# Kernel optimization log

Measured on AMD Instinct MI355X. Metric: run time of the kernel, lower is better.

The kernel has to match this reference:

```python
import jax, jax.numpy as jnp
import numpy as np

H = 512      # hidden_dim
K = 3        # conv_kernel_size
CHUNK = 3    # chunk_size
EPS = 1e-5   # BatchNorm eps


def conv1d(x, w, b, pad):
    # x: (B, Cin, L), w: (Cout, Cin, K)
    y = jax.lax.conv_general_dilated(x, w, (1,), [(pad, pad)],
                                     dimension_numbers=("NCH", "OIH", "NCH"))
    return y + b[None, :, None]


def chunk_indices(seq_lens):
    # static int metadata -> numpy index build (loop over small fixed batch only)
    sl = np.asarray(seq_lens)
    bidx, sidx = [], []
    for b, l in enumerate(sl):
        starts = np.arange(0, int(l) - CHUNK + 1, CHUNK)
        bidx.append(np.full(starts.shape[0], b, dtype=np.int32))
        sidx.append(starts.astype(np.int32))
    return np.concatenate(bidx), np.concatenate(sidx)


def setup_inputs() -> dict:
    key = jax.random.key(0)
    ks = jax.random.split(key, 8)
    B, L = 32, 4096
    x = jax.random.normal(ks[0], (B, L), jnp.float32)
    seq_lens = jax.random.randint(ks[1], (B,), 2048, L + 1)

    def w(k, shape):
        return jax.random.normal(k, shape, jnp.float32) * 0.05

    return {
        "x": x,
        "w0": w(ks[2], (H, 1, K)), "b0": jnp.zeros((H,)), "g0": jnp.ones((H,)), "be0": jnp.zeros((H,)),
        "w1": w(ks[3], (H, H, K)), "b1": jnp.zeros((H,)), "g1": jnp.ones((H,)), "be1": jnp.zeros((H,)),
        "w2": w(ks[4], (H, H, K)), "b2": jnp.zeros((H,)), "g2": jnp.ones((H,)), "be2": jnp.zeros((H,)),
        "pw": w(ks[5], (H, H, CHUNK)), "pb": jnp.zeros((H,)),
        "fw": w(ks[6], (1, H)), "fb": jnp.zeros((1,)),
        "seq_lens": seq_lens,
    }


def reference(x, w0, b0, g0, be0, w1, b1, g1, be1, w2, b2, g2, be2,
              pw, pb, fw, fb, seq_lens):
    inv = np.float32(1.0 / np.sqrt(1.0 + EPS))  # BN eval: mean=0, var=1
    h = x[:, None, :]  # (B, 1, L)
    for (w, b, g, be) in ((w0, b0, g0, be0), (w1, b1, g1, be1), (w2, b2, g2, be2)):
        h = jax.nn.relu(conv1d(h, w, b, pad=1))
        h = (g * inv)[None, :, None] * h + be[None, :, None]
    h = jnp.transpose(h, (0, 2, 1))  # (B, L, H)

    bidx_np, sidx_np = chunk_indices(seq_lens)
    bidx = jnp.asarray(bidx_np)
    sidx = jnp.asarray(sidx_np)
    offs = jnp.arange(CHUNK, dtype=jnp.int32)
    chunks = h[bidx[:, None], sidx[:, None] + offs[None, :], :]  # (N, CHUNK, H)

    # pre_fc_conv over a length-CHUNK window == one GEMM per chunk
    z = jnp.einsum("nth,cht->nc", chunks, pw) + pb  # (N, H)
    logits = jax.nn.relu(z) @ fw.T + fb             # (N, 1)
    return jax.nn.sigmoid(logits)[:, 0]             # (N,)
```

## Files before the change

### kernel.cpp

```cpp
#include <hip/hip_runtime.h>

#define HCH 512
#define LSEQ 4096
#define NB 32
#define KW 3
#define KDIM 1536
#define SPAD 1408
#define INVS 0.9999950000374997f

typedef __attribute__((ext_vector_type(8))) short bf16x8;
typedef __attribute__((ext_vector_type(4))) float f32x4;

__device__ inline unsigned short f2bf(float f) {
  unsigned int u = __float_as_uint(f);
  u += 0x7fffu + ((u >> 16) & 1u);
  return (unsigned short)(u >> 16);
}

__device__ inline void gl_lds16(const void* g, void* l) {
  __builtin_amdgcn_global_load_lds(
      (const __attribute__((address_space(1))) void*)g,
      (__attribute__((address_space(3))) void*)l, 16, 0, 0);
}

__global__ void prep_all(const float* __restrict__ w1, const float* __restrict__ w2,
                         const float* __restrict__ pw, unsigned short* __restrict__ wt,
                         const int* __restrict__ seq_lens, int* __restrict__ cum,
                         float* __restrict__ pz, int nz) {
  int idx = blockIdx.x * 256 + threadIdx.x;
  if (idx < nz) pz[idx] = 0.f;
  if (idx == 0) {
    int acc = 0;
    for (int b = 0; b < NB; b++) {
      cum[b] = acc;
      acc += (seq_lens[b] - KW) / KW + 1;
    }
  }
  if (idx < 3 * HCH * KDIM) {
    int which = idx / (HCH * KDIM);
    int r = idx % (HCH * KDIM);
    int c = r / KDIM;
    int rem = r % KDIM;
    int k = rem / HCH, ci = rem % HCH;
    const float* src = (which == 0) ? w1 : ((which == 1) ? w2 : pw);
    wt[idx] = f2bf(src[c * KDIM + ci * KW + k]);
  }
}

__global__ void layer0(const float* __restrict__ x, const float* __restrict__ w0,
                       const float* __restrict__ b0, const float* __restrict__ g0,
                       const float* __restrict__ be0, unsigned short* __restrict__ h0,
                       const int* __restrict__ seq_q) {
  int tid = threadIdx.x;
  int wave = tid >> 6, lane = tid & 63;
  int pos0 = (blockIdx.x * 4 + wave) * 8;
  int l0 = pos0 & (LSEQ - 1);
  if (l0 >= seq_q[pos0 >> 12] + 2) return;
  int c0 = lane * 8;

  float w[24], bb[8], gg[8], ee[8];
  for (int v = 0; v < 6; v++)
    *reinterpret_cast<float4*>(w + v * 4) = *reinterpret_cast<const float4*>(w0 + c0 * 3 + v * 4);
  for (int v = 0; v < 2; v++) {
    *reinterpret_cast<float4*>(bb + v * 4) = *reinterpret_cast<const float4*>(b0 + c0 + v * 4);
    *reinterpret_cast<float4*>(gg + v * 4) = *reinterpret_cast<const float4*>(g0 + c0 + v * 4);
    *reinterpret_cast<float4*>(ee + v * 4) = *reinterpret_cast<const float4*>(be0 + c0 + v * 4);
  }
  for (int c = 0; c < 8; c++) gg[c] *= INVS;

  const float* xb = x + (size_t)(pos0 - l0);
  for (int pp = 0; pp < 8; pp++) {
    int l = l0 + pp;
    float xm1 = (l > 0) ? xb[l - 1] : 0.f;
    float xc = xb[l];
    float xp1 = (l < LSEQ - 1) ? xb[l + 1] : 0.f;
    unsigned int o[4];
    for (int pq = 0; pq < 4; pq++) {
      unsigned int lo = 0, hi = 0;
      for (int s = 0; s < 2; s++) {
        int c = pq * 2 + s;
        float y = w[c * 3] * xm1 + w[c * 3 + 1] * xc + w[c * 3 + 2] * xp1 + bb[c];
        y = fmaxf(y, 0.f);
        unsigned int u = f2bf(gg[c] * y + ee[c]);
        if (s == 0) lo = u; else hi = u;
      }
      o[pq] = lo | (hi << 16);
    }
    uint4 v4; v4.x = o[0]; v4.y = o[1]; v4.z = o[2]; v4.w = o[3];
    *reinterpret_cast<uint4*>(h0 + (size_t)(pos0 + pp) * HCH + c0) = v4;
  }
}

__global__ __launch_bounds__(256, 2) void conv_gemm(
    const unsigned short* __restrict__ hin,
    const unsigned short* __restrict__ wT,
    const float* __restrict__ bconv, const float* __restrict__ g,
    const float* __restrict__ be,
    unsigned short* __restrict__ hout,
    const unsigned short* __restrict__ zp,
    const int* __restrict__ seq_q, int margin) {
  __shared__ unsigned short As[3 * 128 * 32];
  __shared__ unsigned short Bs[272 * 32];

  int tid = threadIdx.x;
  int wave = tid >> 6, lane = tid & 63;
  int cm = blockIdx.x * 128;
  int ntile = blockIdx.y;
  int b = ntile >> 4;
  int l0 = (ntile & 15) << 8;
  int limit = seq_q[b] + margin;
  if (l0 >= limit) return;
  int wn = wave * 64;
  const size_t hb = (size_t)b * LSEQ * HCH;

  f32x4 acc[8][4] = {};

  int lr = lane >> 2;
  int lc = (lane & 3) * 8;

  const unsigned short* bptr[4];
  for (int t = 0; t < 4; t++) {
    int p = l0 - 1 + (wave * 4 + t) * 16 + lr;
    bptr[t] = (p >= 0 && p < LSEQ) ? (hin + hb + (size_t)p * HCH + lc) : (zp + lc);
  }
  const unsigned short* hptr = zp + lc;
  if (wave == 3 && lane < 8) {
    int p = l0 + 255 + lr;
    hptr = (p < LSEQ) ? (hin + hb + (size_t)p * HCH + lc) : (zp + lc);
  }

  const unsigned short* aptr[6];
  unsigned aoff[6];
  for (int t = 0; t < 6; t++) {
    int s = wave * 6 + t;
    int k = s >> 3, c8 = s & 7;
    aptr[t] = wT + (size_t)(cm + c8 * 16 + lr) * KDIM + k * HCH + lc;
    aoff[t] = (unsigned)(k * 4096 + c8 * 512) * 2;
  }

  for (int it = 0; it < 16; it++) {
    int ci0 = it * 32;
    for (int t = 0; t < 6; t++)
      gl_lds16(aptr[t] + ci0, (char*)As + aoff[t]);
    for (int t = 0; t < 4; t++)
      gl_lds16(bptr[t] + ci0, (char*)Bs + (wave * 4 + t) * 1024);
    if (wave == 3)
      gl_lds16(hptr + ci0, (char*)Bs + 256 * 64);
    __syncthreads();

    int quad = lane >> 4, mr = lane & 15;
    for (int k = 0; k < 3; k++) {
      bf16x8 af[8], bfr[4];
      for (int i = 0; i < 8; i++)
        af[i] = *reinterpret_cast<const bf16x8*>(As + k * 4096 + (i * 16 + mr) * 32 + quad * 8);
      for (int j = 0; j < 4; j++)
        bfr[j] = *reinterpret_cast<const bf16x8*>(Bs + (wn + j * 16 + mr + k) * 32 + quad * 8);
      for (int i = 0; i < 8; i++)
        for (int j = 0; j < 4; j++)
          acc[i][j] = __builtin_amdgcn_mfma_f32_16x16x32_bf16(af[i], bfr[j], acc[i][j], 0, 0, 0);
    }
    __syncthreads();
  }

  int quad = lane >> 4, nn = lane & 15;
  for (int i = 0; i < 8; i++) {
    int c = cm + i * 16 + quad * 4;
    f32x4 bc = *reinterpret_cast<const f32x4*>(bconv + c);
    f32x4 gg = *reinterpret_cast<const f32x4*>(g + c);
    f32x4 bb = *reinterpret_cast<const f32x4*>(be + c);
    for (int j = 0; j < 4; j++) {
      int n = l0 + wn + j * 16 + nn;
      if (n >= limit) continue;
      unsigned long long pack = 0;
      for (int r = 0; r < 4; r++) {
        float y = acc[i][j][r] + bc[r];
        y = fmaxf(y, 0.f);
        unsigned long long u = f2bf(gg[r] * INVS * y + bb[r]);
        pack |= u << (16 * r);
      }
      *reinterpret_cast<unsigned long long*>(hout + hb + (size_t)n * HCH + c) = pack;
    }
  }
}

__global__ __launch_bounds__(256) void chunk_gemm(
    const unsigned short* __restrict__ h2,
    const unsigned short* __restrict__ wTp,
    const float* __restrict__ pb, const float* __restrict__ fw,
    const int* __restrict__ seq_q,
    const int* __restrict__ cum_q,
    float* __restrict__ partial,
    const unsigned short* __restrict__ zp) {
  __shared__ unsigned short As[3 * 128 * 32];
  __shared__ unsigned short Bs[384 * 32];

  int tid = threadIdx.x;
  int wave = tid >> 6, lane = tid & 63;
  int cm = blockIdx.x * 128;
  int b = blockIdx.y / (SPAD / 128);
  int s_base = (blockIdx.y % (SPAD / 128)) * 128;
  int slen = seq_q[b];
  if (3 * s_base + KW > slen) return;
  int p_base = 3 * s_base;
  int wm = (wave >> 1) * 64;
  int wn = (wave & 1) * 64;
  const size_t hb = (size_t)b * LSEQ * HCH;

  f32x4 acc[4][4] = {};

  int lr = lane >> 2, lc = (lane & 3) * 8;

  const unsigned short* bptr[6];
  const unsigned short* aptr[6];
  unsigned aoff[6];
  for (int t = 0; t < 6; t++) {
    int c = wave * 6 + t;
    int p = p_base + c * 16 + lr;
    bptr[t] = (p < LSEQ) ? (h2 + hb + (size_t)p * HCH + lc) : (zp + lc);
    int k = c >> 3, c8 = c & 7;
    aptr[t] = wTp + (size_t)(cm + c8 * 16 + lr) * KDIM + k * HCH + lc;
    aoff[t] = (unsigned)(k * 4096 + c8 * 512) * 2;
  }

  for (int it = 0; it < 16; it++) {
    int ci0 = it * 32;
    for (int t = 0; t < 6; t++) {
      gl_lds16(aptr[t] + ci0, (char*)As + aoff[t]);
      gl_lds16(bptr[t] + ci0, (char*)Bs + (wave * 6 + t) * 1024);
    }
    __syncthreads();

    int quad = lane >> 4, mr = lane & 15;
    for (int t = 0; t < 3; t++) {
      bf16x8 af[4], bfr[4];
      for (int i = 0; i < 4; i++)
        af[i] = *reinterpret_cast<const bf16x8*>(As + t * 4096 + (wm + i * 16 + mr) * 32 + quad * 8);
      for (int j = 0; j < 4; j++)
        bfr[j] = *reinterpret_cast<const bf16x8*>(Bs + (3 * (wn + j * 16 + mr) + t) * 32 + quad * 8);
      for (int i = 0; i < 4; i++)
        for (int j = 0; j < 4; j++)
          acc[i][j] = __builtin_amdgcn_mfma_f32_16x16x32_bf16(af[i], bfr[j], acc[i][j], 0, 0, 0);
    }
    __syncthreads();
  }

  int quad = lane >> 4, nn = lane & 15;
  for (int j = 0; j < 4; j++) {
    float s = 0.f;
    for (int i = 0; i < 4; i++) {
      int c = cm + wm + i * 16 + quad * 4;
      f32x4 pbv = *reinterpret_cast<const f32x4*>(pb + c);
      f32x4 fwv = *reinterpret_cast<const f32x4*>(fw + c);
      for (int r = 0; r < 4; r++) {
        float z = acc[i][j][r] + pbv[r];
        z = fmaxf(z, 0.f);
        s += z * fwv[r];
      }
    }
    s += __shfl_xor(s, 16, 64);
    s += __shfl_xor(s, 32, 64);
    if (quad == 0) {
      int sc = s_base + wn + j * 16 + nn;
      if (3 * sc + KW <= slen) atomicAdd(partial + cum_q[b] + sc, s);
    }
  }
}

__global__ void finalize(const float* __restrict__ partial, const float* __restrict__ fb,
                         float* __restrict__ out, int n) {
  int i = blockIdx.x * 256 + threadIdx.x;
  if (i < n) {
    float t = partial[i] + fb[0];
    out[i] = 1.f / (1.f + expf(-t));
  }
}

extern "C" void kernel_launch(void* const* d_in, const int* in_sizes, int n_in,
                              void* d_out, int out_size, void* d_ws, size_t ws_size,
                              hipStream_t stream) {
  (void)in_sizes; (void)n_in;
  const float* x   = (const float*)d_in[0];
  const float* w0  = (const float*)d_in[1];
  const float* b0  = (const float*)d_in[2];
  const float* g0  = (const float*)d_in[3];
  const float* be0 = (const float*)d_in[4];
  const float* w1  = (const float*)d_in[5];
  const float* b1  = (const float*)d_in[6];
  const float* g1  = (const float*)d_in[7];
  const float* be1 = (const float*)d_in[8];
  const float* w2  = (const float*)d_in[9];
  const float* b2  = (const float*)d_in[10];
  const float* g2  = (const float*)d_in[11];
  const float* be2 = (const float*)d_in[12];
  const float* pw  = (const float*)d_in[13];
  const float* pb  = (const float*)d_in[14];
  const float* fw  = (const float*)d_in[15];
  const float* fb  = (const float*)d_in[16];
  const int* seq_lens = (const int*)d_in[17];

  char* ws = (char*)d_ws;
  unsigned short* zeropage = (unsigned short*)ws;
  float* partial = (float*)(ws + 4096);
  size_t off = 4096 + (size_t)out_size * 4;
  off = (off + 255) & ~(size_t)255;
  int* cum = (int*)(ws + off);
  off += NB * 4;
  off = (off + 255) & ~(size_t)255;
  unsigned short* wt = (unsigned short*)(ws + off);
  off += (size_t)3 * HCH * KDIM * 2;
  off = (off + 255) & ~(size_t)255;
  size_t fixed = off;

  const size_t per_batch = (size_t)LSEQ * HCH * 2;
  int nb_pass = NB;
  while (nb_pass > 1 && fixed + 2 * per_batch * (size_t)nb_pass > ws_size)
    nb_pass >>= 1;
  unsigned short* h0 = (unsigned short*)(ws + fixed);
  unsigned short* h1 = h0 + (size_t)nb_pass * LSEQ * HCH;

  int nzero = 1024 + out_size;
  prep_all<<<(3 * HCH * KDIM) / 256, 256, 0, stream>>>(w1, w2, pw, wt, seq_lens, cum,
                                                       (float*)ws, nzero);

  int npass = NB / nb_pass;
  for (int q = 0; q < npass; q++) {
    const float* xq = x + (size_t)q * nb_pass * LSEQ;
    const int* sq = seq_lens + q * nb_pass;
    layer0<<<nb_pass * (LSEQ / 32), 256, 0, stream>>>(xq, w0, b0, g0, be0, h0, sq);
    conv_gemm<<<dim3(4, nb_pass * 16), 256, 0, stream>>>(h0, wt, b1, g1, be1, h1,
                                                         zeropage, sq, 1);
    conv_gemm<<<dim3(4, nb_pass * 16), 256, 0, stream>>>(h1, wt + (size_t)HCH * KDIM,
                                                         b2, g2, be2, h0, zeropage, sq, 0);
    chunk_gemm<<<dim3(4, nb_pass * (SPAD / 128)), 256, 0, stream>>>(
        h0, wt + (size_t)2 * HCH * KDIM, pb, fw,
        sq, cum + q * nb_pass, partial, zeropage);
  }
  finalize<<<(out_size + 255) / 256, 256, 0, stream>>>(partial, fb, (float*)d_out, out_size);
}
```

Before: 645.2 us.

## Rewrite conv GEMM as 8-wave 256x256 tile with double-buffered swizzled LDS

Replaces the 256-thread conv GEMM with a 512-thread kernel that computes a 256-channel by 256-position tile. Global-to-LDS loads are double-buffered and interleaved with MFMA quarters under fine-grained barriers and vmcnt waits. The LDS layout uses an XOR swizzle to avoid bank conflicts, and MFMA sections raise wave priority. The grid is flattened with an XCD-aware block remap. The shifted conv taps are now loaded as separate K-steps, so the halo rows are re-fetched per tap instead of being reused in LDS. The intent is to hide memory latency and raise MFMA utilization, at the cost of higher LDS and register pressure.

```diff
diff --git a/kernel.cpp b/kernel.cpp
--- a/kernel.cpp
+++ b/kernel.cpp
@@ -7,6 +7,7 @@
 #define KDIM 1536
 #define SPAD 1408
 #define INVS 0.9999950000374997f
+#define NT 24
 
 typedef __attribute__((ext_vector_type(8))) short bf16x8;
 typedef __attribute__((ext_vector_type(4))) float f32x4;
@@ -91,7 +92,50 @@
   }
 }
 
-__global__ __launch_bounds__(256, 2) void conv_gemm(
+#define STAGE_A(Mh, nbuf, tn)                                               \
+  { char* d_ = ldsc + ((nbuf)*4 + (Mh)) * 16384 + w * 1024;                 \
+    gl_lds16(aSrc[Mh][0] + (tn)*64, d_);                                    \
+    gl_lds16(aSrc[Mh][1] + (tn)*64, d_ + 8192); }
+
+#define STAGE_B(Nh, nbuf, tn)                                               \
+  { int k_ = (tn) >> 3, ci0_ = ((tn) & 7) << 6;                             \
+    int p0_ = bRow[Nh][0] + k_, p1_ = bRow[Nh][1] + k_;                     \
+    const unsigned short* s0_ = ((unsigned)p0_ < 4096u)                     \
+        ? hin + hb + (size_t)p0_ * HCH + ci0_ + sslot8 : zp + sslot8;       \
+    const unsigned short* s1_ = ((unsigned)p1_ < 4096u)                     \
+        ? hin + hb + (size_t)p1_ * HCH + ci0_ + sslot8 : zp + sslot8;       \
+    char* d_ = ldsc + ((nbuf)*4 + 2 + (Nh)) * 16384 + w * 1024;             \
+    gl_lds16(s0_, d_); gl_lds16(s1_, d_ + 8192); }
+
+#define LOAD_AF(Mh, buf)                                                    \
+  _Pragma("unroll") for (int i_ = 0; i_ < 4; ++i_)                          \
+  _Pragma("unroll") for (int s_ = 0; s_ < 2; ++s_)                          \
+    af[i_][s_] = *reinterpret_cast<const bf16x8*>(                          \
+        ldsb + ((buf)*4 + (Mh)) * 8192 + (wm + i_*16 + mr) * 64 +           \
+        (((s_*4 + quad) ^ (mr & 7)) << 3));
+
+#define LOAD_BF(Nh, buf)                                                    \
+  _Pragma("unroll") for (int j_ = 0; j_ < 2; ++j_)                          \
+  _Pragma("unroll") for (int s_ = 0; s_ < 2; ++s_)                          \
+    bfv[j_][s_] = *reinterpret_cast<const bf16x8*>(                         \
+        ldsb + ((buf)*4 + 2 + (Nh)) * 8192 + (wn + j_*16 + mr) * 64 +       \
+        (((s_*4 + quad) ^ (mr & 7)) << 3));
+
+#define MFMA_Q(Mh, Nh)                                                      \
+  __builtin_amdgcn_s_setprio(1);                                            \
+  _Pragma("unroll") for (int i_ = 0; i_ < 4; ++i_)                          \
+  _Pragma("unroll") for (int j_ = 0; j_ < 2; ++j_)                          \
+  _Pragma("unroll") for (int s_ = 0; s_ < 2; ++s_)                          \
+    acc[(Mh)*4 + i_][(Nh)*2 + j_] = __builtin_amdgcn_mfma_f32_16x16x32_bf16( \
+        af[i_][s_], bfv[j_][s_], acc[(Mh)*4 + i_][(Nh)*2 + j_], 0, 0, 0);   \
+  __builtin_amdgcn_s_setprio(0);
+
+#define BARRIER { asm volatile("" ::: "memory");                            \
+                  __builtin_amdgcn_s_barrier();                             \
+                  asm volatile("" ::: "memory"); }
+#define WAITV(n) asm volatile("s_waitcnt vmcnt(" #n ")" ::: "memory");
+
+__global__ __launch_bounds__(512, 2) void conv_gemm8(
     const unsigned short* __restrict__ hin,
     const unsigned short* __restrict__ wT,
     const float* __restrict__ bconv, const float* __restrict__ g,
@@ -99,83 +143,94 @@
     unsigned short* __restrict__ hout,
     const unsigned short* __restrict__ zp,
     const int* __restrict__ seq_q, int margin) {
-  __shared__ unsigned short As[3 * 128 * 32];
-  __shared__ unsigned short Bs[272 * 32];
-
-  int tid = threadIdx.x;
-  int wave = tid >> 6, lane = tid & 63;
-  int cm = blockIdx.x * 128;
-  int ntile = blockIdx.y;
-  int b = ntile >> 4;
-  int l0 = (ntile & 15) << 8;
+  __shared__ unsigned short ldsb[8 * 8192];
+
+  int f = blockIdx.x;
+  int cpx = gridDim.x >> 3;
+  int s = (f & 7) * cpx + (f >> 3);
+  int cm = (s & 1) << 8;
+  int y = s >> 1;
+  int b = y >> 4;
+  int l0 = (y & 15) << 8;
   int limit = seq_q[b] + margin;
   if (l0 >= limit) return;
-  int wn = wave * 64;
+
   const size_t hb = (size_t)b * LSEQ * HCH;
+  int tid = threadIdx.x;
+  int w = tid >> 6, lane = tid & 63;
+  int quad = lane >> 4, mr = lane & 15;
+  int wm = (w >> 2) << 6;
+  int wn = (w & 3) << 5;
+  int srow = tid >> 3;
+  int sslot8 = (((tid & 7) ^ (srow & 7)) << 3);
+
+  const unsigned short* aSrc[2][2];
+#pragma unroll
+  for (int Mh = 0; Mh < 2; ++Mh)
+#pragma unroll
+    for (int g2 = 0; g2 < 2; ++g2)
+      aSrc[Mh][g2] = wT + (size_t)(cm + Mh*128 + g2*64 + srow) * KDIM + sslot8;
+  int bRow[2][2];
+#pragma unroll
+  for (int Nh = 0; Nh < 2; ++Nh)
+#pragma unroll
+    for (int g2 = 0; g2 < 2; ++g2)
+      bRow[Nh][g2] = l0 - 1 + Nh*128 + g2*64 + srow;
 
   f32x4 acc[8][4] = {};
-
-  int lr = lane >> 2;
-  int lc = (lane & 3) * 8;
-
-  const unsigned short* bptr[4];
-  for (int t = 0; t < 4; t++) {
-    int p = l0 - 1 + (wave * 4 + t) * 16 + lr;
-    bptr[t] = (p >= 0 && p < LSEQ) ? (hin + hb + (size_t)p * HCH + lc) : (zp + lc);
-  }
-  const unsigned short* hptr = zp + lc;
-  if (wave == 3 && lane < 8) {
-    int p = l0 + 255 + lr;
-    hptr = (p < LSEQ) ? (hin + hb + (size_t)p * HCH + lc) : (zp + lc);
-  }
-
-  const unsigned short* aptr[6];
-  unsigned aoff[6];
-  for (int t = 0; t < 6; t++) {
-    int s = wave * 6 + t;
-    int k = s >> 3, c8 = s & 7;
-    aptr[t] = wT + (size_t)(cm + c8 * 16 + lr) * KDIM + k * HCH + lc;
-    aoff[t] = (unsigned)(k * 4096 + c8 * 512) * 2;
-  }
-
-  for (int it = 0; it < 16; it++) {
-    int ci0 = it * 32;
-    for (int t = 0; t < 6; t++)
-      gl_lds16(aptr[t] + ci0, (char*)As + aoff[t]);
-    for (int t = 0; t < 4; t++)
-      gl_lds16(bptr[t] + ci0, (char*)Bs + (wave * 4 + t) * 1024);
-    if (wave == 3)
-      gl_lds16(hptr + ci0, (char*)Bs + 256 * 64);
-    __syncthreads();
-
-    int quad = lane >> 4, mr = lane & 15;
-    for (int k = 0; k < 3; k++) {
-      bf16x8 af[8], bfr[4];
-      for (int i = 0; i < 8; i++)
-        af[i] = *reinterpret_cast<const bf16x8*>(As + k * 4096 + (i * 16 + mr) * 32 + quad * 8);
-      for (int j = 0; j < 4; j++)
-        bfr[j] = *reinterpret_cast<const bf16x8*>(Bs + (wn + j * 16 + mr + k) * 32 + quad * 8);
-      for (int i = 0; i < 8; i++)
-        for (int j = 0; j < 4; j++)
-          acc[i][j] = __builtin_amdgcn_mfma_f32_16x16x32_bf16(af[i], bfr[j], acc[i][j], 0, 0, 0);
-    }
-    __syncthreads();
-  }
-
-  int quad = lane >> 4, nn = lane & 15;
-  for (int i = 0; i < 8; i++) {
-    int c = cm + i * 16 + quad * 4;
+  char* ldsc = (char*)ldsb;
+
+  STAGE_B(0, 0, 0); STAGE_B(1, 0, 0); STAGE_A(0, 0, 0); STAGE_A(1, 0, 0);
+  WAITV(2);
+  __builtin_amdgcn_s_barrier();
+  asm volatile("" ::: "memory");
+
+#pragma unroll 2
+  for (int t = 0; t < NT; ++t) {
+    int buf = t & 1, nbuf = buf ^ 1;
+    int tn = (t + 1 < NT) ? t + 1 : t;
+    bf16x8 af[4][2], bfv[2][2];
+    LOAD_AF(0, buf); LOAD_BF(0, buf);
+    STAGE_B(0, nbuf, tn); STAGE_B(1, nbuf, tn);
+    BARRIER;
+    MFMA_Q(0, 0);
+    BARRIER;
+    LOAD_BF(1, buf);
+    STAGE_A(0, nbuf, tn);
+    BARRIER;
+    MFMA_Q(0, 1);
+    WAITV(6);
+    BARRIER;
+    LOAD_AF(1, buf); LOAD_BF(0, buf);
+    STAGE_A(1, nbuf, tn);
+    BARRIER;
+    MFMA_Q(1, 0);
+    BARRIER;
+    LOAD_BF(1, buf);
+    BARRIER;
+    MFMA_Q(1, 1);
+    WAITV(2);
+    BARRIER;
+  }
+
+#pragma unroll
+  for (int ai = 0; ai < 8; ++ai) {
+    int Mh = ai >> 2, i = ai & 3;
+    int c = cm + Mh*128 + wm + i*16 + quad*4;
     f32x4 bc = *reinterpret_cast<const f32x4*>(bconv + c);
     f32x4 gg = *reinterpret_cast<const f32x4*>(g + c);
     f32x4 bb = *reinterpret_cast<const f32x4*>(be + c);
-    for (int j = 0; j < 4; j++) {
-      int n = l0 + wn + j * 16 + nn;
+#pragma unroll
+    for (int aj = 0; aj < 4; ++aj) {
+      int Nh = aj >> 1, j = aj & 1;
+      int n = l0 + Nh*128 + wn + j*16 + (lane & 15);
       if (n >= limit) continue;
       unsigned long long pack = 0;
-      for (int r = 0; r < 4; r++) {
-        float y = acc[i][j][r] + bc[r];
-        y = fmaxf(y, 0.f);
-        unsigned long long u = f2bf(gg[r] * INVS * y + bb[r]);
+#pragma unroll
+      for (int r = 0; r < 4; ++r) {
+        float yv = acc[ai][aj][r] + bc[r];
+        yv = fmaxf(yv, 0.f);
+        unsigned long long u = f2bf(gg[r] * INVS * yv + bb[r]);
         pack |= u << (16 * r);
       }
       *reinterpret_cast<unsigned long long*>(hout + hb + (size_t)n * HCH + c) = pack;
@@ -326,11 +381,11 @@
   for (int q = 0; q < npass; q++) {
     const float* xq = x + (size_t)q * nb_pass * LSEQ;
     const int* sq = seq_lens + q * nb_pass;
+    int nwg = nb_pass * 32;
     layer0<<<nb_pass * (LSEQ / 32), 256, 0, stream>>>(xq, w0, b0, g0, be0, h0, sq);
-    conv_gemm<<<dim3(4, nb_pass * 16), 256, 0, stream>>>(h0, wt, b1, g1, be1, h1,
-                                                         zeropage, sq, 1);
-    conv_gemm<<<dim3(4, nb_pass * 16), 256, 0, stream>>>(h1, wt + (size_t)HCH * KDIM,
-                                                         b2, g2, be2, h0, zeropage, sq, 0);
+    conv_gemm8<<<nwg, 512, 0, stream>>>(h0, wt, b1, g1, be1, h1, zeropage, sq, 1);
+    conv_gemm8<<<nwg, 512, 0, stream>>>(h1, wt + (size_t)HCH * KDIM, b2, g2, be2, h0,
+                                        zeropage, sq, 0);
     chunk_gemm<<<dim3(4, nb_pass * (SPAD / 128)), 256, 0, stream>>>(
         h0, wt + (size_t)2 * HCH * KDIM, pb, fw,
         sq, cum + q * nb_pass, partial, zeropage);
```

New measurement: 643.7 us. Within noise of the previous version (-0.2%).
